# Performance work log

Measured on AMD Instinct MI355X. Metric: run time of the kernel, lower is better.

## Reference

```python
import jax, jax.numpy as jnp
import numpy as np

N_NODES = 50000
N_EDGES = 800000
IN_C, HID_C, OUT_C = 256, 512, 256
DROP_P = 0.5


def _glorot(key, fan_in, fan_out):
    lim = float(np.sqrt(6.0 / (fan_in + fan_out)))
    return jax.random.uniform(key, (fan_in, fan_out), jnp.float32, -lim, lim)


def setup_inputs() -> dict:
    key = jax.random.key(0)
    k_x, k_e, k_w1, k_w2 = jax.random.split(key, 4)
    tensor = jax.random.normal(k_x, (N_NODES, IN_C), dtype=jnp.float32)
    edge_index = jax.random.randint(k_e, (2, N_EDGES), 0, N_NODES, dtype=jnp.int64)
    W1 = _glorot(k_w1, IN_C, HID_C)
    b1 = jnp.zeros((HID_C,), jnp.float32)
    W2 = _glorot(k_w2, HID_C, OUT_C)
    b2 = jnp.zeros((OUT_C,), jnp.float32)
    return {"tensor": tensor, "edge_index": edge_index,
            "W1": W1, "b1": b1, "W2": W2, "b2": b2}


def _gcn_conv(x, W, b, row, col, n_nodes):
    # PyG GCNConv: x' = D^-1/2 (A + I) D^-1/2 (x W) + b
    x = x @ W                                            # [N, F_out]
    # degree over targets including self-loops
    deg = jax.ops.segment_sum(jnp.ones_like(col, dtype=x.dtype), col,
                              num_segments=n_nodes) + 1.0
    dinv = jnp.where(deg > 0, jax.lax.rsqrt(deg), 0.0)   # [N]
    norm = dinv[row] * dinv[col]                         # [E]
    msg = x[row] * norm[:, None]                         # [E, F_out] gather
    out = jax.ops.segment_sum(msg, col, num_segments=n_nodes)  # scatter-add
    out = out + x * (dinv * dinv)[:, None]               # self-loop term
    return out + b


def _dropout(x, key, p=DROP_P):
    keep = jax.random.bernoulli(key, 1.0 - p, x.shape)
    return jnp.where(keep, x / (1.0 - p), 0.0)


def reference(tensor, edge_index, W1, b1, W2, b2):
    row, col = edge_index[0], edge_index[1]
    k1, k2 = jax.random.split(jax.random.key(42))
    x = _gcn_conv(tensor, W1, b1, row, col, N_NODES)
    x = _dropout(jax.nn.relu(x), k1)
    x = _gcn_conv(x, W2, b2, row, col, N_NODES)
    x = _dropout(jax.nn.relu(x), k2)
    return x
```

## Files before the change

### kernel.cpp

```cpp
#include <hip/hip_runtime.h>
#include <stdint.h>


#define N_NODES 50000
#define N_EDGES 800000
#define M_PAD   50048
#define IN_C 256
#define HID_C 512
#define OUT_C 256

typedef __attribute__((ext_vector_type(8))) short bf16x8;
typedef __attribute__((ext_vector_type(4))) float f32x4;

struct U2 { unsigned a, b; };

__host__ __device__ constexpr unsigned rotl32(unsigned x, int d) {
  return (x << d) | (x >> (32 - d));
}

#define TF_ROUND(r) { x0 += x1; x1 = rotl32(x1, (r)); x1 ^= x0; }

__host__ __device__ constexpr U2 threefry2x32(unsigned k0, unsigned k1,
                                              unsigned x0, unsigned x1) {
  unsigned ks2 = k0 ^ k1 ^ 0x1BD11BDAu;
  x0 += k0; x1 += k1;
  TF_ROUND(13) TF_ROUND(15) TF_ROUND(26) TF_ROUND(6)  x0 += k1;  x1 += ks2 + 1u;
  TF_ROUND(17) TF_ROUND(29) TF_ROUND(16) TF_ROUND(24) x0 += ks2; x1 += k0 + 2u;
  TF_ROUND(13) TF_ROUND(15) TF_ROUND(26) TF_ROUND(6)  x0 += k0;  x1 += k1 + 3u;
  TF_ROUND(17) TF_ROUND(29) TF_ROUND(16) TF_ROUND(24) x0 += k1;  x1 += ks2 + 4u;
  TF_ROUND(13) TF_ROUND(15) TF_ROUND(26) TF_ROUND(6)  x0 += ks2; x1 += k0 + 5u;
  return U2{x0, x1};
}

__device__ __forceinline__ float drop_apply(float v, unsigned idx, unsigned k0, unsigned k1) {
  v = fmaxf(v, 0.f);
  U2 r = threefry2x32(k0, k1, 0u, idx);
  unsigned bits = r.a ^ r.b;
  return (bits >> 31) ? 0.f : v * 2.0f;
}

__device__ __forceinline__ ushort f2b(float f) {
  unsigned u = __builtin_bit_cast(unsigned, f);
  unsigned r = (u + 0x7fffu + ((u >> 16) & 1u)) >> 16;
  return (ushort)r;
}
__device__ __forceinline__ float b2f(ushort h) {
  unsigned u = (unsigned)h << 16;
  return __builtin_bit_cast(float, u);
}

__device__ __forceinline__ void gload16(const void* g, void* l) {
  __builtin_amdgcn_global_load_lds(
      (const __attribute__((address_space(1))) void*)g,
      (__attribute__((address_space(3))) void*)l, 16, 0, 0);
}

__global__ void deg_kernel(const int* __restrict__ col, int* __restrict__ cnt, int E) {
  int e = blockIdx.x * 256 + threadIdx.x;
  if (e < E) atomicAdd(&cnt[col[e]], 1);
}

__global__ void dinv_kernel(const int* __restrict__ cnt, float* __restrict__ dinv, int N) {
  int n = blockIdx.x * 256 + threadIdx.x;
  if (n < N) dinv[n] = rsqrtf((float)cnt[n] + 1.0f);
}

__global__ __launch_bounds__(1024) void scan_local(const int* __restrict__ cnt,
                                                   int* __restrict__ indptr,
                                                   int* __restrict__ chunkSums, int n) {
  __shared__ int s[1024];
  int gid = blockIdx.x * 1024 + threadIdx.x;
  int v = (gid < n) ? cnt[gid] : 0;
  s[threadIdx.x] = v;
  __syncthreads();
#pragma unroll
  for (int off = 1; off < 1024; off <<= 1) {
    int t = (threadIdx.x >= off) ? s[threadIdx.x - off] : 0;
    __syncthreads();
    s[threadIdx.x] += t;
    __syncthreads();
  }
  if (gid < n) indptr[gid] = s[threadIdx.x] - v;
  if (threadIdx.x == 1023) chunkSums[blockIdx.x] = s[1023];
}

__global__ void scan_chunks(int* __restrict__ chunkSums, int nChunks) {
  if (threadIdx.x == 0 && blockIdx.x == 0) {
    int acc = 0;
    for (int i = 0; i < nChunks; ++i) { int t = chunkSums[i]; chunkSums[i] = acc; acc += t; }
  }
}

__global__ void add_offsets(int* __restrict__ indptr, const int* __restrict__ chunkSums,
                            int n, int total) {
  int gid = blockIdx.x * 256 + threadIdx.x;
  if (gid < n) indptr[gid] += chunkSums[gid >> 10];
  if (gid == 0) indptr[n] = total;
}

__global__ void build_csr(const int* __restrict__ row, const int* __restrict__ col,
                          const int* __restrict__ indptr, int* __restrict__ cursor,
                          const float* __restrict__ dinv,
                          int2* __restrict__ srcW, int E) {
  int e = blockIdx.x * 256 + threadIdx.x;
  if (e < E) {
    int r = row[e];
    int c = col[e];
    int p = indptr[c] + atomicAdd(&cursor[c], 1);
    srcW[p] = make_int2(r, __builtin_bit_cast(int, dinv[r]));
  }
}

__global__ void cvt_f32_bf16(const float* __restrict__ in, ushort* __restrict__ out, int n4) {
  int i = blockIdx.x * 256 + threadIdx.x;
  if (i < n4) {
    float4 v = *(const float4*)(in + (size_t)i * 4);
    ushort4 o = make_ushort4(f2b(v.x), f2b(v.y), f2b(v.z), f2b(v.w));
    *(ushort4*)(out + (size_t)i * 4) = o;
  }
}

template <int LOGK>
__global__ void wT_kernel(const float* __restrict__ W, ushort* __restrict__ WT, int N, int total) {
  int i = blockIdx.x * 256 + threadIdx.x;
  if (i < total) {
    int k = i & ((1 << LOGK) - 1);
    int n = i >> LOGK;
    WT[i] = f2b(W[(size_t)k * N + n]);
  }
}

#define ROW_ACC(vv, ww)                                                        \
  { a0 += b2f((vv).x) * (ww); a1 += b2f((vv).y) * (ww);                        \
    a2 += b2f((vv).z) * (ww); a3 += b2f((vv).w) * (ww); }

template <bool EPI>
__global__ __launch_bounds__(256) void gather_agg16(const ushort* __restrict__ X,
                                                    const int* __restrict__ indptr,
                                                    const int2* __restrict__ srcW,
                                                    const float* __restrict__ dinv,
                                                    const float* __restrict__ bias,
                                                    void* __restrict__ outp,
                                                    unsigned char* __restrict__ maskOut,
                                                    unsigned kk0, unsigned kk1, int N) {
  int wid = (blockIdx.x * 256 + threadIdx.x) >> 6;
  int lane = threadIdx.x & 63;
  if (wid >= N) return;
  int beg = __builtin_amdgcn_readfirstlane(indptr[wid]);
  int end = __builtin_amdgcn_readfirstlane(indptr[wid + 1]);
  float dc = dinv[wid];
  const int f0 = lane * 4;
  ushort4 sv = *(const ushort4*)(X + (size_t)wid * 256 + f0);
  float a0 = b2f(sv.x) * dc, a1 = b2f(sv.y) * dc,
        a2 = b2f(sv.z) * dc, a3 = b2f(sv.w) * dc;

  int e = beg;
  for (; e + 8 <= end; e += 8) {
    int2 p0 = srcW[e + 0], p1 = srcW[e + 1], p2 = srcW[e + 2], p3 = srcW[e + 3];
    int2 p4 = srcW[e + 4], p5 = srcW[e + 5], p6 = srcW[e + 6], p7 = srcW[e + 7];
    ushort4 v0 = *(const ushort4*)(X + (size_t)p0.x * 256 + f0);
    ushort4 v1 = *(const ushort4*)(X + (size_t)p1.x * 256 + f0);
    ushort4 v2 = *(const ushort4*)(X + (size_t)p2.x * 256 + f0);
    ushort4 v3 = *(const ushort4*)(X + (size_t)p3.x * 256 + f0);
    ushort4 v4 = *(const ushort4*)(X + (size_t)p4.x * 256 + f0);
    ushort4 v5 = *(const ushort4*)(X + (size_t)p5.x * 256 + f0);
    ushort4 v6 = *(const ushort4*)(X + (size_t)p6.x * 256 + f0);
    ushort4 v7 = *(const ushort4*)(X + (size_t)p7.x * 256 + f0);
    ROW_ACC(v0, __builtin_bit_cast(float, p0.y));
    ROW_ACC(v1, __builtin_bit_cast(float, p1.y));
    ROW_ACC(v2, __builtin_bit_cast(float, p2.y));
    ROW_ACC(v3, __builtin_bit_cast(float, p3.y));
    ROW_ACC(v4, __builtin_bit_cast(float, p4.y));
    ROW_ACC(v5, __builtin_bit_cast(float, p5.y));
    ROW_ACC(v6, __builtin_bit_cast(float, p6.y));
    ROW_ACC(v7, __builtin_bit_cast(float, p7.y));
  }
  for (; e + 2 <= end; e += 2) {
    int2 p0 = srcW[e + 0], p1 = srcW[e + 1];
    ushort4 v0 = *(const ushort4*)(X + (size_t)p0.x * 256 + f0);
    ushort4 v1 = *(const ushort4*)(X + (size_t)p1.x * 256 + f0);
    ROW_ACC(v0, __builtin_bit_cast(float, p0.y));
    ROW_ACC(v1, __builtin_bit_cast(float, p1.y));
  }
  if (e < end) {
    int2 p0 = srcW[e];
    ushort4 v0 = *(const ushort4*)(X + (size_t)p0.x * 256 + f0);
    ROW_ACC(v0, __builtin_bit_cast(float, p0.y));
  }
  a0 *= dc; a1 *= dc; a2 *= dc; a3 *= dc;

  if (EPI) {
    unsigned base = (unsigned)wid * 256u + (unsigned)f0;
    a0 = drop_apply(a0 + bias[f0 + 0], base + 0, kk0, kk1);
    a1 = drop_apply(a1 + bias[f0 + 1], base + 1, kk0, kk1);
    a2 = drop_apply(a2 + bias[f0 + 2], base + 2, kk0, kk1);
    a3 = drop_apply(a3 + bias[f0 + 3], base + 3, kk0, kk1);
    *(float4*)((float*)outp + (size_t)wid * 256 + f0) = make_float4(a0, a1, a2, a3);
  } else {
    ushort4 o = make_ushort4(f2b(a0), f2b(a1), f2b(a2), f2b(a3));
    *(ushort4*)((ushort*)outp + (size_t)wid * 256 + f0) = o;
    unsigned gl = (unsigned)wid * 64u + (unsigned)lane;
    unsigned eb = gl * 8u;
    unsigned byte = 0;
#pragma unroll
    for (int j = 0; j < 8; ++j) {
      U2 r = threefry2x32(kk0, kk1, 0u, eb + (unsigned)j);
      byte |= (((r.a ^ r.b) >> 31) & 1u) << j;
    }
    maskOut[gl] = (unsigned char)byte;
  }
}

template <bool EPI>
__global__ __launch_bounds__(256) void gemm_bf16(const ushort* __restrict__ A,
                                                 const ushort* __restrict__ BT,
                                                 ushort* __restrict__ C,
                                                 int M, int K, int N,
                                                 const float* __restrict__ bias,
                                                 const unsigned char* __restrict__ mask) {
  __shared__ __align__(16) ushort lds[4 * 128 * 64];
  const int tid = threadIdx.x;
  const int lane = tid & 63;
  const int wv = tid >> 6;
  const int wr = wv >> 1, wc = wv & 1;
  const int bm = blockIdx.x * 128;
  const int bn = blockIdx.y * 128;

  f32x4 acc[4][4] = {};
  const int xorv = (lane & 7) << 4;

  auto stage = [&](int buf, int k0) {
#pragma unroll
    for (int l = 0; l < 4; ++l) {
      int cid = l * 256 + tid;
      int row = cid >> 3;
      int kcol = ((cid & 7) ^ (row & 7)) * 8;
      gload16(A + (size_t)(bm + row) * K + k0 + kcol, (void*)(lds + buf * 8192 + cid * 8));
      gload16(BT + (size_t)(bn + row) * K + k0 + kcol, (void*)(lds + (2 + buf) * 8192 + cid * 8));
    }
  };

  const int nt = K >> 6;
  stage(0, 0);
  __syncthreads();
  int cur = 0;
  for (int t = 0; t < nt; ++t) {
    if (t + 1 < nt) stage(cur ^ 1, (t + 1) << 6);
    const char* Ab = (const char*)(lds + cur * 8192);
    const char* Bb = (const char*)(lds + (2 + cur) * 8192);
#pragma unroll
    for (int ks = 0; ks < 2; ++ks) {
      bf16x8 af[4], bf[4];
      const int kb = (ks * 64 + (lane >> 4) * 16) ^ xorv;
#pragma unroll
      for (int i = 0; i < 4; ++i) {
        int arow = wr * 64 + i * 16 + (lane & 15);
        af[i] = *(const bf16x8*)(Ab + arow * 128 + kb);
        int brow = wc * 64 + i * 16 + (lane & 15);
        bf[i] = *(const bf16x8*)(Bb + brow * 128 + kb);
      }
#pragma unroll
      for (int m = 0; m < 4; ++m)
#pragma unroll
        for (int n = 0; n < 4; ++n)
          acc[m][n] = __builtin_amdgcn_mfma_f32_16x16x32_bf16(af[m], bf[n], acc[m][n], 0, 0, 0);
    }
    __syncthreads();
    cur ^= 1;
  }

  ushort* Csm = (ushort*)lds;
  const int rowoff = wr * 64 + ((lane >> 4) << 2);
  const int coloff = wc * 64 + (lane & 15);
  float bias_v[4];
  if (EPI) {
#pragma unroll
    for (int n = 0; n < 4; ++n) bias_v[n] = bias[bn + coloff + n * 16];
  }
#pragma unroll
  for (int m = 0; m < 4; ++m) {
#pragma unroll
    for (int r = 0; r < 4; ++r) {
      int lrow = rowoff + m * 16 + r;
      unsigned long long mk = 0;
      if (EPI) {
        unsigned base = (unsigned)(bm + lrow) * (unsigned)N + (unsigned)(bn + wc * 64);
        mk = *(const unsigned long long*)(mask + (base >> 3));
      }
#pragma unroll
      for (int n = 0; n < 4; ++n) {
        float v = acc[m][n][r];
        if (EPI) {
          v = fmaxf(v + bias_v[n], 0.f);
          v = ((mk >> ((lane & 15) + n * 16)) & 1ull) ? 0.f : v * 2.0f;
        }
        Csm[lrow * 132 + coloff + n * 16] = f2b(v);
      }
    }
  }
  __syncthreads();
  {
    int row = tid >> 1, ch = (tid & 1) * 64;
    const ushort* src = Csm + row * 132 + ch;
    ushort* dst = C + (size_t)(bm + row) * N + bn + ch;
#pragma unroll
    for (int j = 0; j < 8; ++j)
      *(bf16x8*)(dst + j * 8) = *(const bf16x8*)(src + j * 8);
  }
}

extern "C" void kernel_launch(void* const* d_in, const int* in_sizes, int n_in,
                              void* d_out, int out_size, void* d_ws, size_t ws_size,
                              hipStream_t stream) {
  const float* x  = (const float*)d_in[0];
  const int*   ei = (const int*)d_in[1];
  const float* W1 = (const float*)d_in[2];
  const float* b1 = (const float*)d_in[3];
  const float* W2 = (const float*)d_in[4];
  const float* b2 = (const float*)d_in[5];
  float* out = (float*)d_out;
  (void)in_sizes; (void)n_in; (void)out_size; (void)ws_size;

  const int* row = ei;
  const int* col = ei + N_EDGES;

  char* ws = (char*)d_ws;
  float*  dinv      = (float*) (ws);
  int*    cnt       = (int*)   (ws + (1u << 18));
  int*    indptr    = (int*)   (ws + (2u << 18));
  int*    cursor    = (int*)   (ws + (3u << 18));
  int*    chunkSums = (int*)   (ws + (1u << 20));
  int2*   srcW      = (int2*)  (ws + 2u * (1u << 20));
  ushort* W1T       = (ushort*)(ws + 9u * (1u << 20));
  ushort* W2T       = (ushort*)(ws + 9u * (1u << 20) + (1u << 19));
  unsigned char* mask1 = (unsigned char*)(ws + 10u * (1u << 20));
  ushort* x16       = (ushort*)(ws + 14u * (1u << 20));
  ushort* aggB      = (ushort*)(ws + 40u * (1u << 20));
  ushort* h         = (ushort*)(ws + 66u * (1u << 20));
  ushort* hw2       = (ushort*)(ws + 118u* (1u << 20));

  constexpr U2 K1 = threefry2x32(0u, 42u, 0u, 0u);
  constexpr U2 K2 = threefry2x32(0u, 42u, 0u, 1u);

  hipMemsetAsync(cnt, 0, N_NODES * sizeof(int), stream);
  hipMemsetAsync(cursor, 0, N_NODES * sizeof(int), stream);
  deg_kernel<<<(N_EDGES + 255) / 256, 256, 0, stream>>>(col, cnt, N_EDGES);
  dinv_kernel<<<(N_NODES + 255) / 256, 256, 0, stream>>>(cnt, dinv, N_NODES);
  const int nChunks = (N_NODES + 1023) / 1024;
  scan_local<<<nChunks, 1024, 0, stream>>>(cnt, indptr, chunkSums, N_NODES);
  scan_chunks<<<1, 64, 0, stream>>>(chunkSums, nChunks);
  add_offsets<<<(N_NODES + 255) / 256, 256, 0, stream>>>(indptr, chunkSums, N_NODES, N_EDGES);
  build_csr<<<(N_EDGES + 255) / 256, 256, 0, stream>>>(row, col, indptr, cursor, dinv, srcW, N_EDGES);

  cvt_f32_bf16<<<(N_NODES * IN_C / 4 + 255) / 256, 256, 0, stream>>>(x, x16, N_NODES * IN_C / 4);
  wT_kernel<8><<<(IN_C * HID_C + 255) / 256, 256, 0, stream>>>(W1, W1T, HID_C, IN_C * HID_C);
  wT_kernel<9><<<(HID_C * OUT_C + 255) / 256, 256, 0, stream>>>(W2, W2T, OUT_C, HID_C * OUT_C);
  hipMemsetAsync(aggB + (size_t)N_NODES * IN_C, 0, (size_t)(M_PAD - N_NODES) * IN_C * 2, stream);

  gather_agg16<false><<<(N_NODES + 3) / 4, 256, 0, stream>>>(
      x16, indptr, srcW, dinv, nullptr, aggB, mask1, K1.a, K1.b, N_NODES);
  gemm_bf16<true><<<dim3(M_PAD / 128, HID_C / 128), 256, 0, stream>>>(
      aggB, W1T, h, M_PAD, IN_C, HID_C, b1, mask1);

  gemm_bf16<false><<<dim3(M_PAD / 128, OUT_C / 128), 256, 0, stream>>>(
      h, W2T, hw2, M_PAD, HID_C, OUT_C, nullptr, nullptr);
  gather_agg16<true><<<(N_NODES + 3) / 4, 256, 0, stream>>>(
      hw2, indptr, srcW, dinv, b2, out, nullptr, K2.a, K2.b, N_NODES);
}
```

Measured before the change: 333.4 us.

## Split gather across half-waves with 16-byte loads and move dropout RNG into GEMMs

The aggregation kernel now has each half-wave handle alternate edges, with each lane loading 8 bf16 values (16 bytes) per neighbour row. The two halves are combined with a cross-lane shuffle at the end. Dropout mask generation moves out of the gathers: layer-1 threefry dropout is computed inline in the first GEMM epilogue, and the layer-2 mask bits are computed in the second GEMM and read back by the final gather. This gives wider memory transactions and more loads in flight in the gather, at the cost of heavier RNG work in the GEMM epilogues.

```diff
diff --git a/kernel.cpp b/kernel.cpp
--- a/kernel.cpp
+++ b/kernel.cpp
@@ -44,9 +44,18 @@
   unsigned r = (u + 0x7fffu + ((u >> 16) & 1u)) >> 16;
   return (ushort)r;
 }
-__device__ __forceinline__ float b2f(ushort h) {
-  unsigned u = (unsigned)h << 16;
-  return __builtin_bit_cast(float, u);
+__device__ __forceinline__ float b2f_hi(unsigned u) {
+  return __builtin_bit_cast(float, u & 0xffff0000u);
+}
+__device__ __forceinline__ float b2f_lo(unsigned u) {
+  return __builtin_bit_cast(float, u << 16);
+}
+
+__device__ __forceinline__ void acc8(float (&a)[8], uint4 u, float wgt) {
+  a[0] += b2f_lo(u.x) * wgt; a[1] += b2f_hi(u.x) * wgt;
+  a[2] += b2f_lo(u.y) * wgt; a[3] += b2f_hi(u.y) * wgt;
+  a[4] += b2f_lo(u.z) * wgt; a[5] += b2f_hi(u.z) * wgt;
+  a[6] += b2f_lo(u.w) * wgt; a[7] += b2f_hi(u.w) * wgt;
 }
 
 __device__ __forceinline__ void gload16(const void* g, void* l) {
@@ -130,94 +139,92 @@
   }
 }
 
-#define ROW_ACC(vv, ww)                                                        \
-  { a0 += b2f((vv).x) * (ww); a1 += b2f((vv).y) * (ww);                        \
-    a2 += b2f((vv).z) * (ww); a3 += b2f((vv).w) * (ww); }
-
 template <bool EPI>
-__global__ __launch_bounds__(256) void gather_agg16(const ushort* __restrict__ X,
-                                                    const int* __restrict__ indptr,
-                                                    const int2* __restrict__ srcW,
-                                                    const float* __restrict__ dinv,
-                                                    const float* __restrict__ bias,
-                                                    void* __restrict__ outp,
-                                                    unsigned char* __restrict__ maskOut,
-                                                    unsigned kk0, unsigned kk1, int N) {
+__global__ __launch_bounds__(256) void gather_pair(const ushort* __restrict__ X,
+                                                   const int* __restrict__ indptr,
+                                                   const int2* __restrict__ srcW,
+                                                   const float* __restrict__ dinv,
+                                                   const float* __restrict__ bias,
+                                                   void* __restrict__ outp,
+                                                   const unsigned char* __restrict__ mask2,
+                                                   int N) {
   int wid = (blockIdx.x * 256 + threadIdx.x) >> 6;
   int lane = threadIdx.x & 63;
   if (wid >= N) return;
+  const int sub = lane >> 5;
+  const int fi = lane & 31;
+  const int f0 = fi * 8;
   int beg = __builtin_amdgcn_readfirstlane(indptr[wid]);
   int end = __builtin_amdgcn_readfirstlane(indptr[wid + 1]);
   float dc = dinv[wid];
-  const int f0 = lane * 4;
-  ushort4 sv = *(const ushort4*)(X + (size_t)wid * 256 + f0);
-  float a0 = b2f(sv.x) * dc, a1 = b2f(sv.y) * dc,
-        a2 = b2f(sv.z) * dc, a3 = b2f(sv.w) * dc;
-
-  int e = beg;
-  for (; e + 8 <= end; e += 8) {
-    int2 p0 = srcW[e + 0], p1 = srcW[e + 1], p2 = srcW[e + 2], p3 = srcW[e + 3];
-    int2 p4 = srcW[e + 4], p5 = srcW[e + 5], p6 = srcW[e + 6], p7 = srcW[e + 7];
-    ushort4 v0 = *(const ushort4*)(X + (size_t)p0.x * 256 + f0);
-    ushort4 v1 = *(const ushort4*)(X + (size_t)p1.x * 256 + f0);
-    ushort4 v2 = *(const ushort4*)(X + (size_t)p2.x * 256 + f0);
-    ushort4 v3 = *(const ushort4*)(X + (size_t)p3.x * 256 + f0);
-    ushort4 v4 = *(const ushort4*)(X + (size_t)p4.x * 256 + f0);
-    ushort4 v5 = *(const ushort4*)(X + (size_t)p5.x * 256 + f0);
-    ushort4 v6 = *(const ushort4*)(X + (size_t)p6.x * 256 + f0);
-    ushort4 v7 = *(const ushort4*)(X + (size_t)p7.x * 256 + f0);
-    ROW_ACC(v0, __builtin_bit_cast(float, p0.y));
-    ROW_ACC(v1, __builtin_bit_cast(float, p1.y));
-    ROW_ACC(v2, __builtin_bit_cast(float, p2.y));
-    ROW_ACC(v3, __builtin_bit_cast(float, p3.y));
-    ROW_ACC(v4, __builtin_bit_cast(float, p4.y));
-    ROW_ACC(v5, __builtin_bit_cast(float, p5.y));
-    ROW_ACC(v6, __builtin_bit_cast(float, p6.y));
-    ROW_ACC(v7, __builtin_bit_cast(float, p7.y));
-  }
-  for (; e + 2 <= end; e += 2) {
-    int2 p0 = srcW[e + 0], p1 = srcW[e + 1];
-    ushort4 v0 = *(const ushort4*)(X + (size_t)p0.x * 256 + f0);
-    ushort4 v1 = *(const ushort4*)(X + (size_t)p1.x * 256 + f0);
-    ROW_ACC(v0, __builtin_bit_cast(float, p0.y));
-    ROW_ACC(v1, __builtin_bit_cast(float, p1.y));
-  }
-  if (e < end) {
-    int2 p0 = srcW[e];
-    ushort4 v0 = *(const ushort4*)(X + (size_t)p0.x * 256 + f0);
-    ROW_ACC(v0, __builtin_bit_cast(float, p0.y));
-  }
-  a0 *= dc; a1 *= dc; a2 *= dc; a3 *= dc;
+
+  float a[8] = {};
+  if (sub == 0) {
+    uint4 u = *(const uint4*)(X + (size_t)wid * 256 + f0);
+    acc8(a, u, dc);
+  }
+  int eb = beg;
+  for (; eb + 8 <= end; eb += 8) {
+    int2 q0 = srcW[eb + 0 + sub];
+    int2 q1 = srcW[eb + 2 + sub];
+    int2 q2 = srcW[eb + 4 + sub];
+    int2 q3 = srcW[eb + 6 + sub];
+    uint4 u0 = *(const uint4*)(X + (size_t)q0.x * 256 + f0);
+    uint4 u1 = *(const uint4*)(X + (size_t)q1.x * 256 + f0);
+    uint4 u2 = *(const uint4*)(X + (size_t)q2.x * 256 + f0);
+    uint4 u3 = *(const uint4*)(X + (size_t)q3.x * 256 + f0);
+    acc8(a, u0, __builtin_bit_cast(float, q0.y));
+    acc8(a, u1, __builtin_bit_cast(float, q1.y));
+    acc8(a, u2, __builtin_bit_cast(float, q2.y));
+    acc8(a, u3, __builtin_bit_cast(float, q3.y));
+  }
+  for (int e = eb + sub; e < end; e += 2) {
+    int2 q = srcW[e];
+    uint4 u = *(const uint4*)(X + (size_t)q.x * 256 + f0);
+    acc8(a, u, __builtin_bit_cast(float, q.y));
+  }
+#pragma unroll
+  for (int j = 0; j < 8; ++j) {
+    a[j] += __shfl_xor(a[j], 32);
+    a[j] *= dc;
+  }
 
   if (EPI) {
-    unsigned base = (unsigned)wid * 256u + (unsigned)f0;
-    a0 = drop_apply(a0 + bias[f0 + 0], base + 0, kk0, kk1);
-    a1 = drop_apply(a1 + bias[f0 + 1], base + 1, kk0, kk1);
-    a2 = drop_apply(a2 + bias[f0 + 2], base + 2, kk0, kk1);
-    a3 = drop_apply(a3 + bias[f0 + 3], base + 3, kk0, kk1);
-    *(float4*)((float*)outp + (size_t)wid * 256 + f0) = make_float4(a0, a1, a2, a3);
+    float4 bv0 = *(const float4*)(bias + f0);
+    float4 bv1 = *(const float4*)(bias + f0 + 4);
+    unsigned mk = mask2[(size_t)wid * 32 + fi];
+    float v[8];
+    v[0] = fmaxf(a[0] + bv0.x, 0.f); v[1] = fmaxf(a[1] + bv0.y, 0.f);
+    v[2] = fmaxf(a[2] + bv0.z, 0.f); v[3] = fmaxf(a[3] + bv0.w, 0.f);
+    v[4] = fmaxf(a[4] + bv1.x, 0.f); v[5] = fmaxf(a[5] + bv1.y, 0.f);
+    v[6] = fmaxf(a[6] + bv1.z, 0.f); v[7] = fmaxf(a[7] + bv1.w, 0.f);
+#pragma unroll
+    for (int j = 0; j < 8; ++j) v[j] = ((mk >> j) & 1u) ? 0.f : v[j] * 2.0f;
+    float4 o;
+    if (sub == 0) o = make_float4(v[0], v[1], v[2], v[3]);
+    else          o = make_float4(v[4], v[5], v[6], v[7]);
+    *(float4*)((float*)outp + (size_t)wid * 256 + f0 + sub * 4) = o;
   } else {
-    ushort4 o = make_ushort4(f2b(a0), f2b(a1), f2b(a2), f2b(a3));
-    *(ushort4*)((ushort*)outp + (size_t)wid * 256 + f0) = o;
-    unsigned gl = (unsigned)wid * 64u + (unsigned)lane;
-    unsigned eb = gl * 8u;
-    unsigned byte = 0;
-#pragma unroll
-    for (int j = 0; j < 8; ++j) {
-      U2 r = threefry2x32(kk0, kk1, 0u, eb + (unsigned)j);
-      byte |= (((r.a ^ r.b) >> 31) & 1u) << j;
-    }
-    maskOut[gl] = (unsigned char)byte;
-  }
-}
-
-template <bool EPI>
+    uint2 o;
+    if (sub == 0) {
+      o.x = (unsigned)f2b(a[0]) | ((unsigned)f2b(a[1]) << 16);
+      o.y = (unsigned)f2b(a[2]) | ((unsigned)f2b(a[3]) << 16);
+    } else {
+      o.x = (unsigned)f2b(a[4]) | ((unsigned)f2b(a[5]) << 16);
+      o.y = (unsigned)f2b(a[6]) | ((unsigned)f2b(a[7]) << 16);
+    }
+    *(uint2*)((ushort*)outp + (size_t)wid * 256 + f0 + sub * 4) = o;
+  }
+}
+
+template <int MODE>
 __global__ __launch_bounds__(256) void gemm_bf16(const ushort* __restrict__ A,
                                                  const ushort* __restrict__ BT,
                                                  ushort* __restrict__ C,
                                                  int M, int K, int N,
                                                  const float* __restrict__ bias,
-                                                 const unsigned char* __restrict__ mask) {
+                                                 unsigned char* __restrict__ maskOut,
+                                                 unsigned kk0, unsigned kk1) {
   __shared__ __align__(16) ushort lds[4 * 128 * 64];
   const int tid = threadIdx.x;
   const int lane = tid & 63;
@@ -273,7 +280,7 @@
   const int rowoff = wr * 64 + ((lane >> 4) << 2);
   const int coloff = wc * 64 + (lane & 15);
   float bias_v[4];
-  if (EPI) {
+  if (MODE == 1) {
 #pragma unroll
     for (int n = 0; n < 4; ++n) bias_v[n] = bias[bn + coloff + n * 16];
   }
@@ -282,17 +289,12 @@
 #pragma unroll
     for (int r = 0; r < 4; ++r) {
       int lrow = rowoff + m * 16 + r;
-      unsigned long long mk = 0;
-      if (EPI) {
-        unsigned base = (unsigned)(bm + lrow) * (unsigned)N + (unsigned)(bn + wc * 64);
-        mk = *(const unsigned long long*)(mask + (base >> 3));
-      }
 #pragma unroll
       for (int n = 0; n < 4; ++n) {
         float v = acc[m][n][r];
-        if (EPI) {
-          v = fmaxf(v + bias_v[n], 0.f);
-          v = ((mk >> ((lane & 15) + n * 16)) & 1ull) ? 0.f : v * 2.0f;
+        if (MODE == 1) {
+          unsigned idx = (unsigned)(bm + lrow) * (unsigned)N + (unsigned)(bn + coloff + n * 16);
+          v = drop_apply(v + bias_v[n], idx, kk0, kk1);
         }
         Csm[lrow * 132 + coloff + n * 16] = f2b(v);
       }
@@ -306,6 +308,17 @@
 #pragma unroll
     for (int j = 0; j < 8; ++j)
       *(bf16x8*)(dst + j * 8) = *(const bf16x8*)(src + j * 8);
+    if (MODE == 2) {
+      int grow = bm + row;
+      unsigned base = (unsigned)grow * (unsigned)N + (unsigned)(bn + ch);
+      unsigned long long mword = 0;
+#pragma unroll
+      for (int j = 0; j < 64; ++j) {
+        U2 rr = threefry2x32(kk0, kk1, 0u, base + (unsigned)j);
+        mword |= (unsigned long long)(((rr.a ^ rr.b) >> 31) & 1u) << j;
+      }
+      *(unsigned long long*)(maskOut + (size_t)(base >> 3)) = mword;
+    }
   }
 }
 
@@ -333,7 +346,7 @@
   int2*   srcW      = (int2*)  (ws + 2u * (1u << 20));
   ushort* W1T       = (ushort*)(ws + 9u * (1u << 20));
   ushort* W2T       = (ushort*)(ws + 9u * (1u << 20) + (1u << 19));
-  unsigned char* mask1 = (unsigned char*)(ws + 10u * (1u << 20));
+  unsigned char* mask2 = (unsigned char*)(ws + 10u * (1u << 20));
   ushort* x16       = (ushort*)(ws + 14u * (1u << 20));
   ushort* aggB      = (ushort*)(ws + 40u * (1u << 20));
   ushort* h         = (ushort*)(ws + 66u * (1u << 20));
@@ -342,8 +355,8 @@
   constexpr U2 K1 = threefry2x32(0u, 42u, 0u, 0u);
   constexpr U2 K2 = threefry2x32(0u, 42u, 0u, 1u);
 
-  hipMemsetAsync(cnt, 0, N_NODES * sizeof(int), stream);
-  hipMemsetAsync(cursor, 0, N_NODES * sizeof(int), stream);
+  (void)hipMemsetAsync(cnt, 0, N_NODES * sizeof(int), stream);
+  (void)hipMemsetAsync(cursor, 0, N_NODES * sizeof(int), stream);
   deg_kernel<<<(N_EDGES + 255) / 256, 256, 0, stream>>>(col, cnt, N_EDGES);
   dinv_kernel<<<(N_NODES + 255) / 256, 256, 0, stream>>>(cnt, dinv, N_NODES);
   const int nChunks = (N_NODES + 1023) / 1024;
@@ -355,15 +368,15 @@
   cvt_f32_bf16<<<(N_NODES * IN_C / 4 + 255) / 256, 256, 0, stream>>>(x, x16, N_NODES * IN_C / 4);
   wT_kernel<8><<<(IN_C * HID_C + 255) / 256, 256, 0, stream>>>(W1, W1T, HID_C, IN_C * HID_C);
   wT_kernel<9><<<(HID_C * OUT_C + 255) / 256, 256, 0, stream>>>(W2, W2T, OUT_C, HID_C * OUT_C);
-  hipMemsetAsync(aggB + (size_t)N_NODES * IN_C, 0, (size_t)(M_PAD - N_NODES) * IN_C * 2, stream);
-
-  gather_agg16<false><<<(N_NODES + 3) / 4, 256, 0, stream>>>(
-      x16, indptr, srcW, dinv, nullptr, aggB, mask1, K1.a, K1.b, N_NODES);
-  gemm_bf16<true><<<dim3(M_PAD / 128, HID_C / 128), 256, 0, stream>>>(
-      aggB, W1T, h, M_PAD, IN_C, HID_C, b1, mask1);
-
-  gemm_bf16<false><<<dim3(M_PAD / 128, OUT_C / 128), 256, 0, stream>>>(
-      h, W2T, hw2, M_PAD, HID_C, OUT_C, nullptr, nullptr);
-  gather_agg16<true><<<(N_NODES + 3) / 4, 256, 0, stream>>>(
-      hw2, indptr, srcW, dinv, b2, out, nullptr, K2.a, K2.b, N_NODES);
-}
+  (void)hipMemsetAsync(aggB + (size_t)N_NODES * IN_C, 0, (size_t)(M_PAD - N_NODES) * IN_C * 2, stream);
+
+  gather_pair<false><<<(N_NODES + 3) / 4, 256, 0, stream>>>(
+      x16, indptr, srcW, dinv, nullptr, aggB, nullptr, N_NODES);
+  gemm_bf16<1><<<dim3(M_PAD / 128, HID_C / 128), 256, 0, stream>>>(
+      aggB, W1T, h, M_PAD, IN_C, HID_C, b1, nullptr, K1.a, K1.b);
+
+  gemm_bf16<2><<<dim3(M_PAD / 128, OUT_C / 128), 256, 0, stream>>>(
+      h, W2T, hw2, M_PAD, HID_C, OUT_C, nullptr, mask2, K2.a, K2.b);
+  gather_pair<true><<<(N_NODES + 3) / 4, 256, 0, stream>>>(
+      hw2, indptr, srcW, dinv, b2, out, mask2, N_NODES);
+}
```

Result: slower. 375.1 us (+12.5%).

## Precompute layer-2 dropout mask in GEMM2 and simplify GEMM staging/epilogue

Applied to the files above, without the earlier changes.

The threefry dropout mask for layer 2 is now generated inside the second GEMM kernel as a bitmask. The final gather reads that mask instead of running four threefry hashes per element. The GEMM also drops its double-buffered LDS prefetch in favour of a single buffer with a sync per K-tile. Its epilogue writes output directly from registers through a swapped MFMA operand order, with no LDS transpose. This moves the RNG cost off the latency-bound gather and shrinks LDS use, at the cost of losing load/compute overlap in the GEMM and giving it uncoalesced 8-byte stores.

```diff
diff --git a/kernel.cpp b/kernel.cpp
--- a/kernel.cpp
+++ b/kernel.cpp
@@ -32,13 +32,6 @@
   return U2{x0, x1};
 }
 
-__device__ __forceinline__ float drop_apply(float v, unsigned idx, unsigned k0, unsigned k1) {
-  v = fmaxf(v, 0.f);
-  U2 r = threefry2x32(k0, k1, 0u, idx);
-  unsigned bits = r.a ^ r.b;
-  return (bits >> 31) ? 0.f : v * 2.0f;
-}
-
 __device__ __forceinline__ ushort f2b(float f) {
   unsigned u = __builtin_bit_cast(unsigned, f);
   unsigned r = (u + 0x7fffu + ((u >> 16) & 1u)) >> 16;
@@ -135,14 +128,15 @@
     a2 += b2f((vv).z) * (ww); a3 += b2f((vv).w) * (ww); }
 
 template <bool EPI>
-__global__ __launch_bounds__(256) void gather_agg16(const ushort* __restrict__ X,
-                                                    const int* __restrict__ indptr,
-                                                    const int2* __restrict__ srcW,
-                                                    const float* __restrict__ dinv,
-                                                    const float* __restrict__ bias,
-                                                    void* __restrict__ outp,
-                                                    unsigned char* __restrict__ maskOut,
-                                                    unsigned kk0, unsigned kk1, int N) {
+__global__ __launch_bounds__(256) void gather8(const ushort* __restrict__ X,
+                                               const int* __restrict__ indptr,
+                                               const int2* __restrict__ srcW,
+                                               const float* __restrict__ dinv,
+                                               const float* __restrict__ bias,
+                                               void* __restrict__ outp,
+                                               unsigned char* __restrict__ maskGen,
+                                               const unsigned char* __restrict__ maskUse,
+                                               unsigned kk0, unsigned kk1, int N) {
   int wid = (blockIdx.x * 256 + threadIdx.x) >> 6;
   int lane = threadIdx.x & 63;
   if (wid >= N) return;
@@ -190,15 +184,23 @@
   a0 *= dc; a1 *= dc; a2 *= dc; a3 *= dc;
 
   if (EPI) {
-    unsigned base = (unsigned)wid * 256u + (unsigned)f0;
-    a0 = drop_apply(a0 + bias[f0 + 0], base + 0, kk0, kk1);
-    a1 = drop_apply(a1 + bias[f0 + 1], base + 1, kk0, kk1);
-    a2 = drop_apply(a2 + bias[f0 + 2], base + 2, kk0, kk1);
-    a3 = drop_apply(a3 + bias[f0 + 3], base + 3, kk0, kk1);
-    *(float4*)((float*)outp + (size_t)wid * 256 + f0) = make_float4(a0, a1, a2, a3);
+    float4 bv = *(const float4*)(bias + f0);
+    unsigned mk = maskUse[(size_t)wid * 32 + (lane >> 1)];
+    int sh = (lane & 1) * 4;
+    float v0 = fmaxf(a0 + bv.x, 0.f);
+    float v1 = fmaxf(a1 + bv.y, 0.f);
+    float v2 = fmaxf(a2 + bv.z, 0.f);
+    float v3 = fmaxf(a3 + bv.w, 0.f);
+    v0 = ((mk >> (sh + 0)) & 1u) ? 0.f : v0 * 2.0f;
+    v1 = ((mk >> (sh + 1)) & 1u) ? 0.f : v1 * 2.0f;
+    v2 = ((mk >> (sh + 2)) & 1u) ? 0.f : v2 * 2.0f;
+    v3 = ((mk >> (sh + 3)) & 1u) ? 0.f : v3 * 2.0f;
+    *(float4*)((float*)outp + (size_t)wid * 256 + f0) = make_float4(v0, v1, v2, v3);
   } else {
-    ushort4 o = make_ushort4(f2b(a0), f2b(a1), f2b(a2), f2b(a3));
-    *(ushort4*)((ushort*)outp + (size_t)wid * 256 + f0) = o;
+    uint2 o;
+    o.x = (unsigned)f2b(a0) | ((unsigned)f2b(a1) << 16);
+    o.y = (unsigned)f2b(a2) | ((unsigned)f2b(a3) << 16);
+    *(uint2*)((ushort*)outp + (size_t)wid * 256 + f0) = o;
     unsigned gl = (unsigned)wid * 64u + (unsigned)lane;
     unsigned eb = gl * 8u;
     unsigned byte = 0;
@@ -207,18 +209,20 @@
       U2 r = threefry2x32(kk0, kk1, 0u, eb + (unsigned)j);
       byte |= (((r.a ^ r.b) >> 31) & 1u) << j;
     }
-    maskOut[gl] = (unsigned char)byte;
-  }
-}
-
-template <bool EPI>
+    maskGen[gl] = (unsigned char)byte;
+  }
+}
+
+template <int MODE>
 __global__ __launch_bounds__(256) void gemm_bf16(const ushort* __restrict__ A,
                                                  const ushort* __restrict__ BT,
                                                  ushort* __restrict__ C,
                                                  int M, int K, int N,
                                                  const float* __restrict__ bias,
-                                                 const unsigned char* __restrict__ mask) {
-  __shared__ __align__(16) ushort lds[4 * 128 * 64];
+                                                 const unsigned char* __restrict__ mask1,
+                                                 unsigned char* __restrict__ maskOut,
+                                                 unsigned kk0, unsigned kk1) {
+  __shared__ __align__(16) ushort lds[16384];
   const int tid = threadIdx.x;
   const int lane = tid & 63;
   const int wv = tid >> 6;
@@ -229,25 +233,20 @@
   f32x4 acc[4][4] = {};
   const int xorv = (lane & 7) << 4;
 
-  auto stage = [&](int buf, int k0) {
+  const int nt = K >> 6;
+  for (int t = 0; t < nt; ++t) {
+    const int k0 = t << 6;
 #pragma unroll
     for (int l = 0; l < 4; ++l) {
       int cid = l * 256 + tid;
       int row = cid >> 3;
       int kcol = ((cid & 7) ^ (row & 7)) * 8;
-      gload16(A + (size_t)(bm + row) * K + k0 + kcol, (void*)(lds + buf * 8192 + cid * 8));
-      gload16(BT + (size_t)(bn + row) * K + k0 + kcol, (void*)(lds + (2 + buf) * 8192 + cid * 8));
-    }
-  };
-
-  const int nt = K >> 6;
-  stage(0, 0);
-  __syncthreads();
-  int cur = 0;
-  for (int t = 0; t < nt; ++t) {
-    if (t + 1 < nt) stage(cur ^ 1, (t + 1) << 6);
-    const char* Ab = (const char*)(lds + cur * 8192);
-    const char* Bb = (const char*)(lds + (2 + cur) * 8192);
+      gload16(A + (size_t)(bm + row) * K + k0 + kcol, (void*)(lds + cid * 8));
+      gload16(BT + (size_t)(bn + row) * K + k0 + kcol, (void*)(lds + 8192 + cid * 8));
+    }
+    __syncthreads();
+    const char* Ab = (const char*)lds;
+    const char* Bb = (const char*)(lds + 8192);
 #pragma unroll
     for (int ks = 0; ks < 2; ++ks) {
       bf16x8 af[4], bf[4];
@@ -263,49 +262,56 @@
       for (int m = 0; m < 4; ++m)
 #pragma unroll
         for (int n = 0; n < 4; ++n)
-          acc[m][n] = __builtin_amdgcn_mfma_f32_16x16x32_bf16(af[m], bf[n], acc[m][n], 0, 0, 0);
+          acc[m][n] = __builtin_amdgcn_mfma_f32_16x16x32_bf16(bf[n], af[m], acc[m][n], 0, 0, 0);
     }
     __syncthreads();
-    cur ^= 1;
-  }
-
-  ushort* Csm = (ushort*)lds;
-  const int rowoff = wr * 64 + ((lane >> 4) << 2);
-  const int coloff = wc * 64 + (lane & 15);
-  float bias_v[4];
-  if (EPI) {
-#pragma unroll
-    for (int n = 0; n < 4; ++n) bias_v[n] = bias[bn + coloff + n * 16];
+  }
+
+  const int growb = bm + wr * 64 + (lane & 15);
+  const int gcolb = bn + wc * 64 + ((lane >> 4) << 2);
+  float4 bias_v[4];
+  if (MODE == 1) {
+#pragma unroll
+    for (int n = 0; n < 4; ++n) bias_v[n] = *(const float4*)(bias + gcolb + n * 16);
   }
 #pragma unroll
   for (int m = 0; m < 4; ++m) {
-#pragma unroll
-    for (int r = 0; r < 4; ++r) {
-      int lrow = rowoff + m * 16 + r;
-      unsigned long long mk = 0;
-      if (EPI) {
-        unsigned base = (unsigned)(bm + lrow) * (unsigned)N + (unsigned)(bn + wc * 64);
-        mk = *(const unsigned long long*)(mask + (base >> 3));
+    int grow = growb + m * 16;
+    unsigned long long mrow = 0;
+    if (MODE == 1)
+      mrow = *(const unsigned long long*)(mask1 + (((size_t)grow * N + bn + wc * 64) >> 3));
+#pragma unroll
+    for (int n = 0; n < 4; ++n) {
+      int gcol = gcolb + n * 16;
+      float v[4];
+#pragma unroll
+      for (int r = 0; r < 4; ++r) {
+        float x = acc[m][n][r];
+        if (MODE == 1) {
+          x = fmaxf(x + ((const float*)&bias_v[n])[r], 0.f);
+          int bit = (gcol - (bn + wc * 64)) + r;
+          x = ((mrow >> bit) & 1ull) ? 0.f : x * 2.0f;
+        }
+        v[r] = x;
       }
-#pragma unroll
-      for (int n = 0; n < 4; ++n) {
-        float v = acc[m][n][r];
-        if (EPI) {
-          v = fmaxf(v + bias_v[n], 0.f);
-          v = ((mk >> ((lane & 15) + n * 16)) & 1ull) ? 0.f : v * 2.0f;
-        }
-        Csm[lrow * 132 + coloff + n * 16] = f2b(v);
-      }
-    }
-  }
-  __syncthreads();
-  {
+      uint2 o;
+      o.x = (unsigned)f2b(v[0]) | ((unsigned)f2b(v[1]) << 16);
+      o.y = (unsigned)f2b(v[2]) | ((unsigned)f2b(v[3]) << 16);
+      *(uint2*)(C + (size_t)grow * N + gcol) = o;
+    }
+  }
+
+  if (MODE == 2) {
     int row = tid >> 1, ch = (tid & 1) * 64;
-    const ushort* src = Csm + row * 132 + ch;
-    ushort* dst = C + (size_t)(bm + row) * N + bn + ch;
-#pragma unroll
-    for (int j = 0; j < 8; ++j)
-      *(bf16x8*)(dst + j * 8) = *(const bf16x8*)(src + j * 8);
+    int grow = bm + row;
+    unsigned base = (unsigned)grow * (unsigned)N + (unsigned)(bn + ch);
+    unsigned long long mword = 0;
+#pragma unroll
+    for (int j = 0; j < 64; ++j) {
+      U2 rr = threefry2x32(kk0, kk1, 0u, base + (unsigned)j);
+      mword |= (unsigned long long)(((rr.a ^ rr.b) >> 31) & 1u) << j;
+    }
+    *(unsigned long long*)(maskOut + (size_t)(base >> 3)) = mword;
   }
 }
 
@@ -334,16 +340,17 @@
   ushort* W1T       = (ushort*)(ws + 9u * (1u << 20));
   ushort* W2T       = (ushort*)(ws + 9u * (1u << 20) + (1u << 19));
   unsigned char* mask1 = (unsigned char*)(ws + 10u * (1u << 20));
-  ushort* x16       = (ushort*)(ws + 14u * (1u << 20));
-  ushort* aggB      = (ushort*)(ws + 40u * (1u << 20));
-  ushort* h         = (ushort*)(ws + 66u * (1u << 20));
-  ushort* hw2       = (ushort*)(ws + 118u* (1u << 20));
+  unsigned char* mask2 = (unsigned char*)(ws + 14u * (1u << 20));
+  ushort* x16       = (ushort*)(ws + 18u * (1u << 20));
+  ushort* aggB      = (ushort*)(ws + 44u * (1u << 20));
+  ushort* h         = (ushort*)(ws + 70u * (1u << 20));
+  ushort* hw2       = (ushort*)(ws + 122u* (1u << 20));
 
   constexpr U2 K1 = threefry2x32(0u, 42u, 0u, 0u);
   constexpr U2 K2 = threefry2x32(0u, 42u, 0u, 1u);
 
-  hipMemsetAsync(cnt, 0, N_NODES * sizeof(int), stream);
-  hipMemsetAsync(cursor, 0, N_NODES * sizeof(int), stream);
+  (void)hipMemsetAsync(cnt, 0, N_NODES * sizeof(int), stream);
+  (void)hipMemsetAsync(cursor, 0, N_NODES * sizeof(int), stream);
   deg_kernel<<<(N_EDGES + 255) / 256, 256, 0, stream>>>(col, cnt, N_EDGES);
   dinv_kernel<<<(N_NODES + 255) / 256, 256, 0, stream>>>(cnt, dinv, N_NODES);
   const int nChunks = (N_NODES + 1023) / 1024;
@@ -355,15 +362,15 @@
   cvt_f32_bf16<<<(N_NODES * IN_C / 4 + 255) / 256, 256, 0, stream>>>(x, x16, N_NODES * IN_C / 4);
   wT_kernel<8><<<(IN_C * HID_C + 255) / 256, 256, 0, stream>>>(W1, W1T, HID_C, IN_C * HID_C);
   wT_kernel<9><<<(HID_C * OUT_C + 255) / 256, 256, 0, stream>>>(W2, W2T, OUT_C, HID_C * OUT_C);
-  hipMemsetAsync(aggB + (size_t)N_NODES * IN_C, 0, (size_t)(M_PAD - N_NODES) * IN_C * 2, stream);
-
-  gather_agg16<false><<<(N_NODES + 3) / 4, 256, 0, stream>>>(
-      x16, indptr, srcW, dinv, nullptr, aggB, mask1, K1.a, K1.b, N_NODES);
-  gemm_bf16<true><<<dim3(M_PAD / 128, HID_C / 128), 256, 0, stream>>>(
-      aggB, W1T, h, M_PAD, IN_C, HID_C, b1, mask1);
-
-  gemm_bf16<false><<<dim3(M_PAD / 128, OUT_C / 128), 256, 0, stream>>>(
-      h, W2T, hw2, M_PAD, HID_C, OUT_C, nullptr, nullptr);
-  gather_agg16<true><<<(N_NODES + 3) / 4, 256, 0, stream>>>(
-      hw2, indptr, srcW, dinv, b2, out, nullptr, K2.a, K2.b, N_NODES);
-}
+  (void)hipMemsetAsync(aggB + (size_t)N_NODES * IN_C, 0, (size_t)(M_PAD - N_NODES) * IN_C * 2, stream);
+
+  gather8<false><<<(N_NODES + 3) / 4, 256, 0, stream>>>(
+      x16, indptr, srcW, dinv, nullptr, aggB, mask1, nullptr, K1.a, K1.b, N_NODES);
+  gemm_bf16<1><<<dim3(M_PAD / 128, HID_C / 128), 256, 0, stream>>>(
+      aggB, W1T, h, M_PAD, IN_C, HID_C, b1, mask1, nullptr, 0u, 0u);
+
+  gemm_bf16<2><<<dim3(M_PAD / 128, OUT_C / 128), 256, 0, stream>>>(
+      h, W2T, hw2, M_PAD, HID_C, OUT_C, nullptr, nullptr, mask2, K2.a, K2.b);
+  gather8<true><<<(N_NODES + 3) / 4, 256, 0, stream>>>(
+      hw2, indptr, srcW, dinv, b2, out, nullptr, mask2, 0u, 0u, N_NODES);
+}
```

Result: slower. 350.0 us (+5.0%).
